# Optimization experiments

Measured on AMD Instinct MI355X. Metric: run time of the kernel, lower is better.

Reference implementation:

```python
import jax, jax.numpy as jnp
import numpy as np

B, S, H, L = 16, 512, 768, 4096

def setup_inputs() -> dict:
    key = jax.random.key(0)
    k1, k2, k3 = jax.random.split(key, 3)
    inputs = jax.random.normal(k1, (B, S, H), dtype=jnp.float32)
    # realistic variable-length masks: each sequence has length in [S//2, S]
    lengths = jax.random.randint(k2, (B,), S // 2, S + 1)
    masks = jnp.arange(S)[None, :] < lengths[:, None]  # [B, S] bool
    # xavier_uniform for Linear(H, L, bias=False): weight shape [L, H]
    limit = float(np.sqrt(6.0 / (H + L)))
    W = jax.random.uniform(k3, (L, H), minval=-limit, maxval=limit, dtype=jnp.float32)
    return {"inputs": inputs, "masks": masks, "W": W}

def reference(inputs, masks, W):
    # scores: Linear(inputs) -> [B,S,L], transposed to [B,L,S]
    scores = jnp.einsum("bsh,lh->bls", inputs, W)
    scores = jnp.where(masks[:, None, :], scores, -jnp.inf)
    attn = jax.nn.softmax(scores, axis=-1)  # over seq dim
    # weighted sum pooling: [B,L,S] @ [B,S,H] -> [B,L,H]
    return jnp.einsum("bls,bsh->blh", attn, inputs)
```

## Files before the change

### kernel.cpp

```cpp
#include <hip/hip_runtime.h>
#include <hip/hip_bf16.h>

#define Bn 16
#define Sn 512
#define Hn 768
#define Ln 4096

typedef __attribute__((ext_vector_type(8))) short bf16x8;
typedef __attribute__((ext_vector_type(4))) float f32x4;

using bf16 = __hip_bfloat16;

constexpr int BL = 64;
constexpr int KH = 32;
constexpr int NH = 128;
constexpr int KS = 32;
constexpr int XP = KH + 8;
constexpr int TP = KS + 8;
constexpr int PP = Sn + 8;

union Pack8 { bf16 h[8]; uint4 u; };

__device__ inline uint4 cvt8(float4 a, float4 b) {
  Pack8 p;
  p.h[0] = __float2bfloat16(a.x); p.h[1] = __float2bfloat16(a.y);
  p.h[2] = __float2bfloat16(a.z); p.h[3] = __float2bfloat16(a.w);
  p.h[4] = __float2bfloat16(b.x); p.h[5] = __float2bfloat16(b.y);
  p.h[6] = __float2bfloat16(b.z); p.h[7] = __float2bfloat16(b.w);
  return p.u;
}

__global__ __launch_bounds__(256) void convert_x_kernel(
    const float* __restrict__ X, bf16* __restrict__ Xbf, bf16* __restrict__ XT) {
  __shared__ bf16 t[64][72];
  const int tid = threadIdx.x;
  const int b  = blockIdx.z;
  const int s0 = blockIdx.y * 64;
  const int h0 = blockIdx.x * 64;
  const int r = tid >> 2;
  const int p = tid & 3;
  const float* src = X + ((size_t)b * Sn + s0 + r) * Hn + h0 + p * 16;
  float4 a0 = *(const float4*)(src + 0);
  float4 a1 = *(const float4*)(src + 4);
  float4 a2 = *(const float4*)(src + 8);
  float4 a3 = *(const float4*)(src + 12);
  uint4 u0 = cvt8(a0, a1);
  uint4 u1 = cvt8(a2, a3);
  bf16* xb = Xbf + ((size_t)b * Sn + s0 + r) * Hn + h0 + p * 16;
  *(uint4*)(xb)     = u0;
  *(uint4*)(xb + 8) = u1;
  *(uint4*)&t[r][p * 16]     = u0;
  *(uint4*)&t[r][p * 16 + 8] = u1;
  __syncthreads();
  Pack8 o0, o1;
#pragma unroll
  for (int i = 0; i < 8; ++i) {
    o0.h[i] = t[p * 16 + i][r];
    o1.h[i] = t[p * 16 + 8 + i][r];
  }
  bf16* xt = XT + ((size_t)b * Hn + h0 + r) * Sn + s0 + p * 16;
  *(uint4*)(xt)     = o0.u;
  *(uint4*)(xt + 8) = o1.u;
}

__global__ __launch_bounds__(256) void convert_w_kernel(
    const float* __restrict__ W, bf16* __restrict__ Wbf) {
  const size_t i = ((size_t)blockIdx.x * 256 + threadIdx.x) * 8;
  float4 a0 = *(const float4*)(W + i);
  float4 a1 = *(const float4*)(W + i + 4);
  *(uint4*)(Wbf + i) = cvt8(a0, a1);
}

__global__ __launch_bounds__(256, 2) void attn_main_kernel(
    const int* __restrict__ masks,
    const bf16* __restrict__ Xbf, const bf16* __restrict__ XTg,
    const bf16* __restrict__ Wbf, float* __restrict__ out) {
  __shared__ float bias[Sn];
  __shared__ union {
    struct { bf16 Xs[Sn][XP]; bf16 Ws[BL][XP]; } p2;
    struct { bf16 P[BL][PP];  bf16 XT[NH][TP]; } p5;
  } sm;
  const int tid  = threadIdx.x;
  const int wv   = tid >> 6;
  const int lane = tid & 63;
  const int col  = lane & 15;
  const int quad = lane >> 4;
  const int b  = blockIdx.x / (Ln / BL);
  const int l0 = (blockIdx.x % (Ln / BL)) * BL;
  const int r4    = tid & 3;
  const int row64 = tid >> 2;

  for (int i = tid; i < Sn; i += 256)
    bias[i] = masks[b * Sn + i] ? 0.0f : -1e30f;

  const f32x4 zero = {0.f, 0.f, 0.f, 0.f};
  f32x4 acc[32];
#pragma unroll
  for (int i = 0; i < 32; ++i) acc[i] = zero;

  for (int k0 = 0; k0 < Hn; k0 += KH) {
    __syncthreads();
#pragma unroll
    for (int s8 = 0; s8 < 8; ++s8) {
      const int row = s8 * 64 + row64;
      uint4 v = *(const uint4*)(Xbf + ((size_t)b * Sn + row) * Hn + k0 + r4 * 8);
      *(uint4*)&sm.p2.Xs[row][r4 * 8] = v;
    }
    {
      uint4 v = *(const uint4*)(Wbf + (size_t)(l0 + row64) * Hn + k0 + r4 * 8);
      *(uint4*)&sm.p2.Ws[row64][r4 * 8] = v;
    }
    __syncthreads();
    bf16x8 af = *(const bf16x8*)&sm.p2.Ws[wv * 16 + col][quad * 8];
#pragma unroll
    for (int nt = 0; nt < 32; ++nt) {
      bf16x8 bfr = *(const bf16x8*)&sm.p2.Xs[nt * 16 + col][quad * 8];
      acc[nt] = __builtin_amdgcn_mfma_f32_16x16x32_bf16(af, bfr, acc[nt], 0, 0, 0);
    }
  }
  __syncthreads();

  float mx[4] = {-3e38f, -3e38f, -3e38f, -3e38f};
#pragma unroll
  for (int nt = 0; nt < 32; ++nt) {
    const float bi = bias[nt * 16 + col];
#pragma unroll
    for (int r = 0; r < 4; ++r) {
      acc[nt][r] += bi;
      mx[r] = fmaxf(mx[r], acc[nt][r]);
    }
  }
#pragma unroll
  for (int r = 0; r < 4; ++r) {
    mx[r] = fmaxf(mx[r], __shfl_xor(mx[r], 1, 64));
    mx[r] = fmaxf(mx[r], __shfl_xor(mx[r], 2, 64));
    mx[r] = fmaxf(mx[r], __shfl_xor(mx[r], 4, 64));
    mx[r] = fmaxf(mx[r], __shfl_xor(mx[r], 8, 64));
  }
  float sum[4] = {0.f, 0.f, 0.f, 0.f};
#pragma unroll
  for (int nt = 0; nt < 32; ++nt) {
#pragma unroll
    for (int r = 0; r < 4; ++r) {
      const float e = __expf(acc[nt][r] - mx[r]);
      acc[nt][r] = e;
      sum[r] += e;
    }
  }
#pragma unroll
  for (int r = 0; r < 4; ++r) {
    sum[r] += __shfl_xor(sum[r], 1, 64);
    sum[r] += __shfl_xor(sum[r], 2, 64);
    sum[r] += __shfl_xor(sum[r], 4, 64);
    sum[r] += __shfl_xor(sum[r], 8, 64);
  }
  float rs[4];
#pragma unroll
  for (int r = 0; r < 4; ++r) rs[r] = 1.0f / sum[r];

#pragma unroll
  for (int nt = 0; nt < 32; ++nt)
#pragma unroll
    for (int r = 0; r < 4; ++r)
      sm.p5.P[wv * 16 + quad * 4 + r][nt * 16 + col] = __float2bfloat16(acc[nt][r]);
  __syncthreads();

  for (int n0 = 0; n0 < Hn; n0 += NH) {
    f32x4 oacc[8];
#pragma unroll
    for (int i = 0; i < 8; ++i) oacc[i] = zero;
    for (int s0 = 0; s0 < Sn; s0 += KS) {
      __syncthreads();
#pragma unroll
      for (int h2 = 0; h2 < 2; ++h2) {
        const int hrow = h2 * 64 + row64;
        uint4 v = *(const uint4*)(XTg + ((size_t)b * Hn + n0 + hrow) * Sn + s0 + r4 * 8);
        *(uint4*)&sm.p5.XT[hrow][r4 * 8] = v;
      }
      __syncthreads();
      bf16x8 af = *(const bf16x8*)&sm.p5.P[wv * 16 + col][s0 + quad * 8];
#pragma unroll
      for (int nt = 0; nt < 8; ++nt) {
        bf16x8 bfr = *(const bf16x8*)&sm.p5.XT[nt * 16 + col][quad * 8];
        oacc[nt] = __builtin_amdgcn_mfma_f32_16x16x32_bf16(af, bfr, oacc[nt], 0, 0, 0);
      }
    }
#pragma unroll
    for (int nt = 0; nt < 8; ++nt)
#pragma unroll
      for (int r = 0; r < 4; ++r) {
        const int l = l0 + wv * 16 + quad * 4 + r;
        const int h = n0 + nt * 16 + col;
        out[((size_t)b * Ln + l) * Hn + h] = oacc[nt][r] * rs[r];
      }
  }
}

__global__ __launch_bounds__(256) void attn_fallback_kernel(
    const float* __restrict__ X, const int* __restrict__ masks,
    const float* __restrict__ W, float* __restrict__ out) {
  __shared__ float sc[4][Sn];
  const int wv = threadIdx.x >> 6, lane = threadIdx.x & 63;
  const int gw = blockIdx.x * 4 + wv;
  const int b = gw / Ln, l = gw % Ln;
  float wreg[12];
#pragma unroll
  for (int j = 0; j < 12; ++j) wreg[j] = W[(size_t)l * Hn + j * 64 + lane];
  for (int s = 0; s < Sn; ++s) {
    const float* xr = X + ((size_t)b * Sn + s) * Hn;
    float p = 0.f;
#pragma unroll
    for (int j = 0; j < 12; ++j) p += xr[j * 64 + lane] * wreg[j];
#pragma unroll
    for (int off = 32; off > 0; off >>= 1) p += __shfl_xor(p, off, 64);
    if (lane == 0) sc[wv][s] = p;
  }
  __syncthreads();
  float m = -3e38f;
#pragma unroll
  for (int i = 0; i < 8; ++i) {
    const int s = lane * 8 + i;
    const float v = sc[wv][s] + (masks[b * Sn + s] ? 0.f : -1e30f);
    sc[wv][s] = v;
    m = fmaxf(m, v);
  }
#pragma unroll
  for (int off = 32; off > 0; off >>= 1) m = fmaxf(m, __shfl_xor(m, off, 64));
  __syncthreads();
  float sum = 0.f;
#pragma unroll
  for (int i = 0; i < 8; ++i) {
    const int s = lane * 8 + i;
    const float e = __expf(sc[wv][s] - m);
    sc[wv][s] = e;
    sum += e;
  }
#pragma unroll
  for (int off = 32; off > 0; off >>= 1) sum += __shfl_xor(sum, off, 64);
  const float rs = 1.0f / sum;
  __syncthreads();
  float o[12];
#pragma unroll
  for (int j = 0; j < 12; ++j) o[j] = 0.f;
  for (int s = 0; s < Sn; ++s) {
    const float p = sc[wv][s];
    const float* xr = X + ((size_t)b * Sn + s) * Hn;
#pragma unroll
    for (int j = 0; j < 12; ++j) o[j] += p * xr[j * 64 + lane];
  }
#pragma unroll
  for (int j = 0; j < 12; ++j)
    out[((size_t)b * Ln + l) * Hn + j * 64 + lane] = o[j] * rs;
}

extern "C" void kernel_launch(void* const* d_in, const int* in_sizes, int n_in,
                              void* d_out, int out_size, void* d_ws, size_t ws_size,
                              hipStream_t stream) {
  const float* X     = (const float*)d_in[0];
  const int*   masks = (const int*)d_in[1];
  const float* W     = (const float*)d_in[2];
  float* out = (float*)d_out;

  const size_t need = ((size_t)2 * Bn * Sn * Hn + (size_t)Ln * Hn) * sizeof(bf16);
  if (ws_size >= need) {
    bf16* Xbf = (bf16*)d_ws;
    bf16* XT  = Xbf + (size_t)Bn * Sn * Hn;
    bf16* Wbf = XT  + (size_t)Bn * Sn * Hn;
    convert_x_kernel<<<dim3(Hn / 64, Sn / 64, Bn), 256, 0, stream>>>(X, Xbf, XT);
    convert_w_kernel<<<dim3((Ln * Hn) / 2048), 256, 0, stream>>>(W, Wbf);
    attn_main_kernel<<<dim3(Bn * (Ln / BL)), 256, 0, stream>>>(masks, Xbf, XT, Wbf, out);
  } else {
    attn_fallback_kernel<<<dim3(Bn * Ln / 4), 256, 0, stream>>>(X, masks, W, out);
  }
}
```

Measured before the change: 413.9 us.

## Use 2x2 wave tiling, direct global-to-LDS loads, and swizzled LDS layouts

Repartitions the fused attention-pooling kernel so each wave covers 32 L-rows by half of S, or half of an H-tile, instead of 16 rows by everything. Each B fragment read from LDS now feeds two MFMAs. The per-block softmax now needs a cross-wave max/sum reduction through shared memory. Tiles move from global memory straight into LDS via global_load_lds, and XOR-swizzled layouts replace padding to avoid bank conflicts. Masks are held in registers, the P tile is packed to bf16 through lane shuffles, and the PV stage uses larger S steps. Risks include higher register pressure and whether the swizzle and reduction indexing are correct.

```diff
diff --git a/kernel.cpp b/kernel.cpp
--- a/kernel.cpp
+++ b/kernel.cpp
@@ -12,12 +12,28 @@
 using bf16 = __hip_bfloat16;
 
 constexpr int BL = 64;
-constexpr int KH = 32;
-constexpr int NH = 128;
-constexpr int KS = 32;
-constexpr int XP = KH + 8;
-constexpr int TP = KS + 8;
-constexpr int PP = Sn + 8;
+
+constexpr int SM_BYTES = 81920;
+constexpr int XS_OFF   = 0;
+constexpr int WS_OFF   = 32768;
+constexpr int P_OFF    = 0;
+constexpr int XT_OFF   = 65536;
+constexpr int REDM_OFF = 65536;
+constexpr int REDS_OFF = 66048;
+
+typedef const __attribute__((address_space(1))) unsigned int* gas_ptr;
+typedef __attribute__((address_space(3))) unsigned int* las_ptr;
+
+__device__ __forceinline__ void gld_lds16(const void* g, void* l) {
+  __builtin_amdgcn_global_load_lds((gas_ptr)g, (las_ptr)l, 16, 0, 0);
+}
+
+__device__ __forceinline__ unsigned short bfbits(float x) {
+  __hip_bfloat16 h = __float2bfloat16(x);
+  unsigned short u;
+  __builtin_memcpy(&u, &h, 2);
+  return u;
+}
 
 union Pack8 { bf16 h[8]; uint4 u; };
 
@@ -75,123 +91,204 @@
     const int* __restrict__ masks,
     const bf16* __restrict__ Xbf, const bf16* __restrict__ XTg,
     const bf16* __restrict__ Wbf, float* __restrict__ out) {
-  __shared__ float bias[Sn];
-  __shared__ union {
-    struct { bf16 Xs[Sn][XP]; bf16 Ws[BL][XP]; } p2;
-    struct { bf16 P[BL][PP];  bf16 XT[NH][TP]; } p5;
-  } sm;
+  __shared__ char sm[SM_BYTES];
   const int tid  = threadIdx.x;
-  const int wv   = tid >> 6;
+  const int w    = tid >> 6;
   const int lane = tid & 63;
   const int col  = lane & 15;
   const int quad = lane >> 4;
+  const int lg   = w >> 1;
+  const int sg   = w & 1;
   const int b  = blockIdx.x / (Ln / BL);
   const int l0 = (blockIdx.x % (Ln / BL)) * BL;
-  const int r4    = tid & 3;
-  const int row64 = tid >> 2;
-
-  for (int i = tid; i < Sn; i += 256)
-    bias[i] = masks[b * Sn + i] ? 0.0f : -1e30f;
+
+  float bias_r[16];
+  {
+    const int* mrow = masks + b * Sn + sg * 256 + col;
+#pragma unroll
+    for (int nt = 0; nt < 16; ++nt)
+      bias_r[nt] = mrow[nt * 16] ? 0.0f : -1e30f;
+  }
 
   const f32x4 zero = {0.f, 0.f, 0.f, 0.f};
-  f32x4 acc[32];
-#pragma unroll
-  for (int i = 0; i < 32; ++i) acc[i] = zero;
-
-  for (int k0 = 0; k0 < Hn; k0 += KH) {
+  f32x4 acc[2][16];
+#pragma unroll
+  for (int a = 0; a < 2; ++a)
+#pragma unroll
+    for (int nt = 0; nt < 16; ++nt) acc[a][nt] = zero;
+
+  for (int k0 = 0; k0 < Hn; k0 += 32) {
     __syncthreads();
-#pragma unroll
-    for (int s8 = 0; s8 < 8; ++s8) {
-      const int row = s8 * 64 + row64;
-      uint4 v = *(const uint4*)(Xbf + ((size_t)b * Sn + row) * Hn + k0 + r4 * 8);
-      *(uint4*)&sm.p2.Xs[row][r4 * 8] = v;
-    }
     {
-      uint4 v = *(const uint4*)(Wbf + (size_t)(l0 + row64) * Hn + k0 + r4 * 8);
-      *(uint4*)&sm.p2.Ws[row64][r4 * 8] = v;
+      const int r0 = w * 128;
+      const bf16* g = Xbf + ((size_t)b * Sn + r0 + (lane >> 2)) * Hn + k0 + (lane & 3) * 8;
+#pragma unroll
+      for (int i = 0; i < 8; ++i) {
+        gld_lds16(g, &sm[XS_OFF + (r0 + i * 16) * 64]);
+        g += 16 * Hn;
+      }
+      const bf16* gw = Wbf + ((size_t)(l0 + w * 16 + (lane >> 2))) * Hn + k0 + (lane & 3) * 8;
+      gld_lds16(gw, &sm[WS_OFF + (w * 16) * 64]);
     }
     __syncthreads();
-    bf16x8 af = *(const bf16x8*)&sm.p2.Ws[wv * 16 + col][quad * 8];
-#pragma unroll
-    for (int nt = 0; nt < 32; ++nt) {
-      bf16x8 bfr = *(const bf16x8*)&sm.p2.Xs[nt * 16 + col][quad * 8];
-      acc[nt] = __builtin_amdgcn_mfma_f32_16x16x32_bf16(af, bfr, acc[nt], 0, 0, 0);
-    }
-  }
-  __syncthreads();
-
-  float mx[4] = {-3e38f, -3e38f, -3e38f, -3e38f};
-#pragma unroll
-  for (int nt = 0; nt < 32; ++nt) {
-    const float bi = bias[nt * 16 + col];
+    bf16x8 a0 = *(const bf16x8*)&sm[WS_OFF + (lg * 32 + col) * 64 + quad * 16];
+    bf16x8 a1 = *(const bf16x8*)&sm[WS_OFF + (lg * 32 + 16 + col) * 64 + quad * 16];
+#pragma unroll
+    for (int nt = 0; nt < 16; ++nt) {
+      bf16x8 bf_ = *(const bf16x8*)&sm[XS_OFF + (sg * 256 + nt * 16 + col) * 64 + quad * 16];
+      acc[0][nt] = __builtin_amdgcn_mfma_f32_16x16x32_bf16(a0, bf_, acc[0][nt], 0, 0, 0);
+      acc[1][nt] = __builtin_amdgcn_mfma_f32_16x16x32_bf16(a1, bf_, acc[1][nt], 0, 0, 0);
+    }
+  }
+
+  float* redm = (float*)&sm[REDM_OFF];
+  float* reds = (float*)&sm[REDS_OFF];
+  float mx[2][4];
+#pragma unroll
+  for (int a = 0; a < 2; ++a)
+#pragma unroll
+    for (int r = 0; r < 4; ++r) mx[a][r] = -3e38f;
+#pragma unroll
+  for (int a = 0; a < 2; ++a)
+#pragma unroll
+    for (int nt = 0; nt < 16; ++nt)
+#pragma unroll
+      for (int r = 0; r < 4; ++r) {
+        acc[a][nt][r] += bias_r[nt];
+        mx[a][r] = fmaxf(mx[a][r], acc[a][nt][r]);
+      }
+#pragma unroll
+  for (int a = 0; a < 2; ++a)
 #pragma unroll
     for (int r = 0; r < 4; ++r) {
-      acc[nt][r] += bi;
-      mx[r] = fmaxf(mx[r], acc[nt][r]);
-    }
-  }
-#pragma unroll
-  for (int r = 0; r < 4; ++r) {
-    mx[r] = fmaxf(mx[r], __shfl_xor(mx[r], 1, 64));
-    mx[r] = fmaxf(mx[r], __shfl_xor(mx[r], 2, 64));
-    mx[r] = fmaxf(mx[r], __shfl_xor(mx[r], 4, 64));
-    mx[r] = fmaxf(mx[r], __shfl_xor(mx[r], 8, 64));
-  }
-  float sum[4] = {0.f, 0.f, 0.f, 0.f};
-#pragma unroll
-  for (int nt = 0; nt < 32; ++nt) {
+      mx[a][r] = fmaxf(mx[a][r], __shfl_xor(mx[a][r], 1, 64));
+      mx[a][r] = fmaxf(mx[a][r], __shfl_xor(mx[a][r], 2, 64));
+      mx[a][r] = fmaxf(mx[a][r], __shfl_xor(mx[a][r], 4, 64));
+      mx[a][r] = fmaxf(mx[a][r], __shfl_xor(mx[a][r], 8, 64));
+    }
+  if (col == 0) {
+#pragma unroll
+    for (int a = 0; a < 2; ++a)
+#pragma unroll
+      for (int r = 0; r < 4; ++r)
+        redm[sg * 64 + lg * 32 + a * 16 + quad * 4 + r] = mx[a][r];
+  }
+  __syncthreads();
+  float gmax[2][4], sum[2][4];
+#pragma unroll
+  for (int a = 0; a < 2; ++a)
 #pragma unroll
     for (int r = 0; r < 4; ++r) {
-      const float e = __expf(acc[nt][r] - mx[r]);
-      acc[nt][r] = e;
-      sum[r] += e;
-    }
-  }
-#pragma unroll
-  for (int r = 0; r < 4; ++r) {
-    sum[r] += __shfl_xor(sum[r], 1, 64);
-    sum[r] += __shfl_xor(sum[r], 2, 64);
-    sum[r] += __shfl_xor(sum[r], 4, 64);
-    sum[r] += __shfl_xor(sum[r], 8, 64);
-  }
-  float rs[4];
-#pragma unroll
-  for (int r = 0; r < 4; ++r) rs[r] = 1.0f / sum[r];
-
-#pragma unroll
-  for (int nt = 0; nt < 32; ++nt)
-#pragma unroll
-    for (int r = 0; r < 4; ++r)
-      sm.p5.P[wv * 16 + quad * 4 + r][nt * 16 + col] = __float2bfloat16(acc[nt][r]);
-  __syncthreads();
-
-  for (int n0 = 0; n0 < Hn; n0 += NH) {
-    f32x4 oacc[8];
-#pragma unroll
-    for (int i = 0; i < 8; ++i) oacc[i] = zero;
-    for (int s0 = 0; s0 < Sn; s0 += KS) {
+      const int row = lg * 32 + a * 16 + quad * 4 + r;
+      gmax[a][r] = fmaxf(redm[row], redm[64 + row]);
+      sum[a][r] = 0.f;
+    }
+#pragma unroll
+  for (int a = 0; a < 2; ++a)
+#pragma unroll
+    for (int nt = 0; nt < 16; ++nt)
+#pragma unroll
+      for (int r = 0; r < 4; ++r) {
+        const float e = __expf(acc[a][nt][r] - gmax[a][r]);
+        acc[a][nt][r] = e;
+        sum[a][r] += e;
+      }
+#pragma unroll
+  for (int a = 0; a < 2; ++a)
+#pragma unroll
+    for (int r = 0; r < 4; ++r) {
+      sum[a][r] += __shfl_xor(sum[a][r], 1, 64);
+      sum[a][r] += __shfl_xor(sum[a][r], 2, 64);
+      sum[a][r] += __shfl_xor(sum[a][r], 4, 64);
+      sum[a][r] += __shfl_xor(sum[a][r], 8, 64);
+    }
+  if (col == 0) {
+#pragma unroll
+    for (int a = 0; a < 2; ++a)
+#pragma unroll
+      for (int r = 0; r < 4; ++r)
+        reds[sg * 64 + lg * 32 + a * 16 + quad * 4 + r] = sum[a][r];
+  }
+  __syncthreads();
+  float rs[2][4];
+#pragma unroll
+  for (int a = 0; a < 2; ++a)
+#pragma unroll
+    for (int r = 0; r < 4; ++r) {
+      const int row = lg * 32 + a * 16 + quad * 4 + r;
+      rs[a][r] = 1.0f / (reds[row] + reds[64 + row]);
+    }
+
+  const int pi = col & 1;
+#pragma unroll
+  for (int a = 0; a < 2; ++a)
+#pragma unroll
+    for (int t = 0; t < 8; ++t)
+#pragma unroll
+      for (int r = 0; r < 4; ++r) {
+        const float own0 = acc[a][2 * t][r];
+        const float own1 = acc[a][2 * t + 1][r];
+        const float p0 = __shfl_xor(own0, 1, 64);
+        const float p1 = __shfl_xor(own1, 1, 64);
+        const float lo = pi ? p1 : own0;
+        const float hi = pi ? own1 : p0;
+        const unsigned pk = (unsigned)bfbits(lo) | ((unsigned)bfbits(hi) << 16);
+        const int nt_w = 2 * t + pi;
+        const int row = lg * 32 + a * 16 + quad * 4 + r;
+        const int sp = sg * 256 + nt_w * 16 + (col & ~1);
+        const int slot = (sp >> 3) ^ (row & 7);
+        *(unsigned*)&sm[P_OFF + row * 1024 + slot * 16 + (sp & 7) * 2] = pk;
+      }
+
+  for (int n0 = 0; n0 < Hn / 128; ++n0) {
+    f32x4 oacc[2][4];
+#pragma unroll
+    for (int a = 0; a < 2; ++a)
+#pragma unroll
+      for (int nt = 0; nt < 4; ++nt) oacc[a][nt] = zero;
+    for (int s0 = 0; s0 < Sn; s0 += 64) {
       __syncthreads();
-#pragma unroll
-      for (int h2 = 0; h2 < 2; ++h2) {
-        const int hrow = h2 * 64 + row64;
-        uint4 v = *(const uint4*)(XTg + ((size_t)b * Hn + n0 + hrow) * Sn + s0 + r4 * 8);
-        *(uint4*)&sm.p5.XT[hrow][r4 * 8] = v;
+      {
+        const int r0 = w * 32;
+        const int rr = lane >> 3;
+        const int cc = lane & 7;
+        const bf16* g = XTg + ((size_t)b * Hn + n0 * 128 + r0 + rr) * Sn + s0 + (cc ^ rr) * 8;
+#pragma unroll
+        for (int i = 0; i < 4; ++i) {
+          gld_lds16(g, &sm[XT_OFF + (r0 + i * 8) * 128]);
+          g += 8 * Sn;
+        }
       }
       __syncthreads();
-      bf16x8 af = *(const bf16x8*)&sm.p5.P[wv * 16 + col][s0 + quad * 8];
-#pragma unroll
-      for (int nt = 0; nt < 8; ++nt) {
-        bf16x8 bfr = *(const bf16x8*)&sm.p5.XT[nt * 16 + col][quad * 8];
-        oacc[nt] = __builtin_amdgcn_mfma_f32_16x16x32_bf16(af, bfr, oacc[nt], 0, 0, 0);
-      }
-    }
-#pragma unroll
-    for (int nt = 0; nt < 8; ++nt)
-#pragma unroll
-      for (int r = 0; r < 4; ++r) {
-        const int l = l0 + wv * 16 + quad * 4 + r;
-        const int h = n0 + nt * 16 + col;
-        out[((size_t)b * Ln + l) * Hn + h] = oacc[nt][r] * rs[r];
+#pragma unroll
+      for (int ks = 0; ks < 2; ++ks) {
+        const int chunk = (s0 + ks * 32 + quad * 8) >> 3;
+        bf16x8 pa[2];
+#pragma unroll
+        for (int a = 0; a < 2; ++a) {
+          const int row = lg * 32 + a * 16 + col;
+          const int slot = chunk ^ (row & 7);
+          pa[a] = *(const bf16x8*)&sm[P_OFF + row * 1024 + slot * 16];
+        }
+#pragma unroll
+        for (int nt = 0; nt < 4; ++nt) {
+          const int hl = (nt * 2 + sg) * 16 + col;
+          const int xslot = (ks * 4 + quad) ^ (hl & 7);
+          bf16x8 xb = *(const bf16x8*)&sm[XT_OFF + hl * 128 + xslot * 16];
+          oacc[0][nt] = __builtin_amdgcn_mfma_f32_16x16x32_bf16(pa[0], xb, oacc[0][nt], 0, 0, 0);
+          oacc[1][nt] = __builtin_amdgcn_mfma_f32_16x16x32_bf16(pa[1], xb, oacc[1][nt], 0, 0, 0);
+        }
+      }
+    }
+#pragma unroll
+    for (int a = 0; a < 2; ++a)
+#pragma unroll
+      for (int nt = 0; nt < 4; ++nt) {
+        const int h = n0 * 128 + (nt * 2 + sg) * 16 + col;
+        const int lbase = l0 + lg * 32 + a * 16 + quad * 4;
+#pragma unroll
+        for (int r = 0; r < 4; ++r)
+          out[((size_t)b * Ln + lbase + r) * Hn + h] = oacc[a][nt][r] * rs[a][r];
       }
   }
 }
```

Measured after the change: 370.8 us. 10.4% less time.
